# Performance work log

Hardware: AMD Instinct MI355X
Metric: run time of the kernel (lower is better)

The kernel has to match this reference:

```python
import jax, jax.numpy as jnp
import numpy as np

B, IN, OUT, K = 16384, 2048, 2048, 8
P, Q = OUT // K, IN // K
W_BIT, IN_BIT = 8, 8
V_MAX = 2.0
ACT_THRES = 6.0


def _ste(base, quantized):
    # straight-through estimator: forward = quantized, backward = d(base)
    return base + jax.lax.stop_gradient(quantized - base)


def quantize_input(x, in_bit):
    # unsigned uniform quantization of activations into [0, 1]
    levels = float(2 ** in_bit - 1)
    xc = jnp.clip(x, 0.0, 1.0)
    xq = jnp.round(xc * levels) / levels
    return _ste(xc, xq)


def quantize_weight(w, w_bit, v_max):
    # symmetric uniform quantization into [-v_max, v_max]
    s = float(2 ** (w_bit - 1) - 1)
    wc = jnp.clip(w, -v_max, v_max)
    wq = jnp.round(wc / v_max * s) / s * v_max
    return _ste(wc, wq)


def setup_inputs() -> dict:
    key = jax.random.key(0)
    k1, k2 = jax.random.split(key)
    x = jax.random.uniform(k1, (B, IN), dtype=jnp.float32)
    weight = jax.random.normal(k2, (P, Q, K, K), dtype=jnp.float32) * 0.1
    return {"x": x, "weight": weight}


def reference(x, weight):
    xq = quantize_input(x, IN_BIT)                    # [B, IN]
    wq = quantize_weight(weight, W_BIT, V_MAX)        # [P, Q, K, K]
    xb = xq.reshape(x.shape[0], Q, K)                 # [B, Q, K]
    # blocked matmul: out[b,p,o] = sum_q sum_i W[p,q,o,i] * x[b,q,i]
    out = jnp.einsum("bqi,pqoi->bpo", xb, wq).reshape(x.shape[0], OUT)
    out = out * out                                   # photodetect: intensity |.|^2
    out = jnp.clip(out, 0.0, ACT_THRES)               # ReLUN(6)
    return out
```

## Files before the change

kernel.cpp:

```cpp
#include <hip/hip_runtime.h>
#include <stdint.h>


typedef int i32x4  __attribute__((ext_vector_type(4)));
typedef int i32x16 __attribute__((ext_vector_type(16)));

#define B_DIM   16384
#define IN_DIM  2048
#define OUT_DIM 2048

#define BM 256
#define BN 256
#define BK 128
#define KTILES (IN_DIM / BK)
#define ATILE  (BM * BK)
#define BUFB   (2 * ATILE)

__device__ __forceinline__ void async16(const void* g, void* l) {
    __builtin_amdgcn_global_load_lds(
        (const __attribute__((address_space(1))) void*)g,
        (__attribute__((address_space(3))) void*)l, 16, 0, 0);
}

__global__ __launch_bounds__(256) void quant_x_kernel(const float* __restrict__ x,
                                                      int8_t* __restrict__ xq) {
    int i = blockIdx.x * 256 + threadIdx.x;
    const float4* xv = (const float4*)x + (size_t)i * 4;
    union { int8_t c[16]; i32x4 v; } u;
#pragma unroll
    for (int j = 0; j < 4; ++j) {
        float4 v = xv[j];
        float f[4] = {v.x, v.y, v.z, v.w};
#pragma unroll
        for (int e = 0; e < 4; ++e) {
            float c = fminf(fmaxf(f[e], 0.0f), 1.0f);
            int q = (int)rintf(c * 255.0f) - 128;
            u.c[j * 4 + e] = (int8_t)q;
        }
    }
    *((i32x4*)xq + i) = u.v;
}

__global__ __launch_bounds__(256) void quant_w_kernel(const float* __restrict__ w,
                                                      int8_t* __restrict__ wq,
                                                      int* __restrict__ rowsum) {
    int p = blockIdx.x;
    int t = threadIdx.x;
    const float* wp = w + (size_t)p * 16384;
    int n = p * 8 + (t & 7);
    int lsum = 0;
#pragma unroll
    for (int s = 0; s < 8; ++s) {
        int g = t + s * 256;
        float4 v0 = *(const float4*)(wp + g * 8);
        float4 v1 = *(const float4*)(wp + g * 8 + 4);
        float f[8] = {v0.x, v0.y, v0.z, v0.w, v1.x, v1.y, v1.z, v1.w};
        union { int8_t c[8]; long long ll; } u;
#pragma unroll
        for (int e = 0; e < 8; ++e) {
            float c = fminf(fmaxf(f[e], -2.0f), 2.0f);
            int q = (int)rintf(c * 63.5f);
            u.c[e] = (int8_t)q;
            lsum += q;
        }
        int kg = g >> 3;
        *(long long*)(wq + (size_t)n * 2048 + kg * 8) = u.ll;
    }
    atomicAdd(&rowsum[n], lsum);
}

#define LD(p) (*(const i32x4*)(p))
#define MFMA32(a, b, c) __builtin_amdgcn_mfma_i32_32x32x32_i8(a, b, c, 0, 0, 0)

__global__ __launch_bounds__(512, 2) void gemm_i8_kernel(const int8_t* __restrict__ A,
                                                         const int8_t* __restrict__ W,
                                                         const int* __restrict__ rowsum,
                                                         float* __restrict__ out) {
    extern __shared__ int8_t lds[];

    int bid = blockIdx.x;
    int wg = (bid & 7) * 64 + (bid >> 3);
    int tm = wg >> 3;
    int tn = wg & 7;
    int browG = tm * BM;
    int bcolG = tn * BN;

    int tid  = threadIdx.x;
    int lane = tid & 63;
    int wv   = tid >> 6;
    int wr = wv >> 2, wc = wv & 3;
    int l31 = lane & 31;
    int hi  = lane >> 5;

    int csw = (tid & 7) ^ ((tid >> 4) & 7);
    const int8_t* gA = A + (size_t)(browG + (tid >> 3)) * IN_DIM + csw * 16;
    const int8_t* gB = W + (size_t)(bcolG + (tid >> 3)) * IN_DIM + csw * 16;
    const int t16 = tid * 16;

    const int xsw = (l31 >> 1) & 7;
    int kof[4];
#pragma unroll
    for (int ks = 0; ks < 4; ++ks)
        kof[ks] = (((2 * ks + hi) ^ xsw) << 4);
    const int arowO = (wr * 128 + l31) * BK;
    const int browO = (wc * 64 + l31) * BK;

    i32x16 acc[4][2];
#pragma unroll
    for (int m = 0; m < 4; ++m)
#pragma unroll
        for (int n = 0; n < 2; ++n)
            acc[m][n] = (i32x16){0, 0, 0, 0, 0, 0, 0, 0, 0, 0, 0, 0, 0, 0, 0, 0};

    async16(gA, lds + t16);
    async16(gA + 131072, lds + 8192 + t16);
    async16(gA + 262144, lds + 16384 + t16);
    async16(gA + 393216, lds + 24576 + t16);
    async16(gB, lds + ATILE + t16);
    async16(gB + 131072, lds + ATILE + 8192 + t16);
    async16(gB + 262144, lds + ATILE + 16384 + t16);
    async16(gB + 393216, lds + ATILE + 24576 + t16);
    __syncthreads();

#pragma unroll 1
    for (int kt = 0; kt < KTILES; ++kt) {
        const int cur = kt & 1;
        const int8_t* la = lds + cur * BUFB;
        const int8_t* lb = la + ATILE;

        if (kt < KTILES - 1) {
            int8_t* dst = lds + (cur ^ 1) * BUFB;
            const int kb = (kt + 1) * BK;
            async16(gA + kb, dst + t16);
            async16(gA + 131072 + kb, dst + 8192 + t16);
            async16(gA + 262144 + kb, dst + 16384 + t16);
            async16(gA + 393216 + kb, dst + 24576 + t16);
            async16(gB + kb, dst + ATILE + t16);
            async16(gB + 131072 + kb, dst + ATILE + 8192 + t16);
            async16(gB + 262144 + kb, dst + ATILE + 16384 + t16);
            async16(gB + 393216 + kb, dst + ATILE + 24576 + t16);
        }

#pragma unroll
        for (int ks = 0; ks < 4; ++ks) {
            i32x4 a0 = LD(la + arowO + kof[ks]);
            i32x4 a1 = LD(la + arowO + 4096 + kof[ks]);
            i32x4 a2 = LD(la + arowO + 8192 + kof[ks]);
            i32x4 a3 = LD(la + arowO + 12288 + kof[ks]);
            i32x4 b0 = LD(lb + browO + kof[ks]);
            i32x4 b1 = LD(lb + browO + 4096 + kof[ks]);
            acc[0][0] = MFMA32(a0, b0, acc[0][0]);
            acc[0][1] = MFMA32(a0, b1, acc[0][1]);
            acc[1][0] = MFMA32(a1, b0, acc[1][0]);
            acc[1][1] = MFMA32(a1, b1, acc[1][1]);
            acc[2][0] = MFMA32(a2, b0, acc[2][0]);
            acc[2][1] = MFMA32(a2, b1, acc[2][1]);
            acc[3][0] = MFMA32(a3, b0, acc[3][0]);
            acc[3][1] = MFMA32(a3, b1, acc[3][1]);
        }
        __syncthreads();
    }

    const float scale = (float)(2.0 / 32385.0);
#pragma unroll
    for (int n = 0; n < 2; ++n) {
        int col = bcolG + wc * 64 + n * 32 + l31;
        int rs128 = rowsum[col] << 7;
#pragma unroll
        for (int m = 0; m < 4; ++m) {
            int rb = browG + wr * 128 + m * 32 + hi * 4;
#pragma unroll
            for (int r = 0; r < 16; ++r) {
                int row = rb + (r & 3) + 8 * (r >> 2);
                float f = (float)(acc[m][n][r] + rs128) * scale;
                f = f * f;
                f = fminf(f, 6.0f);
                out[(size_t)row * OUT_DIM + col] = f;
            }
        }
    }
}

extern "C" void kernel_launch(void* const* d_in, const int* in_sizes, int n_in,
                              void* d_out, int out_size, void* d_ws, size_t ws_size,
                              hipStream_t stream) {
    const float* x  = (const float*)d_in[0];
    const float* wt = (const float*)d_in[1];
    float* out = (float*)d_out;

    char* ws = (char*)d_ws;
    int8_t* xq = (int8_t*)ws;
    int8_t* wq = (int8_t*)(ws + (size_t)B_DIM * IN_DIM);
    int*    rowsum = (int*)(ws + (size_t)B_DIM * IN_DIM
                               + (size_t)OUT_DIM * IN_DIM);

    hipMemsetAsync(rowsum, 0, OUT_DIM * sizeof(int), stream);
    quant_x_kernel<<<(B_DIM * IN_DIM / 16) / 256, 256, 0, stream>>>(x, xq);
    quant_w_kernel<<<256, 256, 0, stream>>>(wt, wq, rowsum);
    gemm_i8_kernel<<<(B_DIM / BM) * (OUT_DIM / BN), 512, 2 * BUFB, stream>>>(xq, wq, rowsum, out);
}
```

Before: 124.9 us.

## Load weight operand directly into registers from pre-swizzled global layout

Result: slower. 129.3 us (+3.6%).

```diff
diff --git a/kernel.cpp b/kernel.cpp
--- a/kernel.cpp
+++ b/kernel.cpp
@@ -14,7 +14,7 @@
 #define BK 128
 #define KTILES (IN_DIM / BK)
 #define ATILE  (BM * BK)
-#define BUFB   (2 * ATILE)
+#define BUFB   ATILE
 
 __device__ __forceinline__ void async16(const void* g, void* l) {
     __builtin_amdgcn_global_load_lds(
@@ -42,13 +42,13 @@
 }
 
 __global__ __launch_bounds__(256) void quant_w_kernel(const float* __restrict__ w,
-                                                      int8_t* __restrict__ wq,
+                                                      int8_t* __restrict__ wqT,
                                                       int* __restrict__ rowsum) {
     int p = blockIdx.x;
     int t = threadIdx.x;
     const float* wp = w + (size_t)p * 16384;
+    int lsum = 0;
     int n = p * 8 + (t & 7);
-    int lsum = 0;
 #pragma unroll
     for (int s = 0; s < 8; ++s) {
         int g = t + s * 256;
@@ -63,8 +63,7 @@
             u.c[e] = (int8_t)q;
             lsum += q;
         }
-        int kg = g >> 3;
-        *(long long*)(wq + (size_t)n * 2048 + kg * 8) = u.ll;
+        *(long long*)(wqT + ((size_t)(g >> 4) << 15) + n * 16 + ((g >> 3) & 1) * 8) = u.ll;
     }
     atomicAdd(&rowsum[n], lsum);
 }
@@ -73,7 +72,7 @@
 #define MFMA32(a, b, c) __builtin_amdgcn_mfma_i32_32x32x32_i8(a, b, c, 0, 0, 0)
 
 __global__ __launch_bounds__(512, 2) void gemm_i8_kernel(const int8_t* __restrict__ A,
-                                                         const int8_t* __restrict__ W,
+                                                         const int8_t* __restrict__ WT,
                                                          const int* __restrict__ rowsum,
                                                          float* __restrict__ out) {
     extern __shared__ int8_t lds[];
@@ -94,7 +93,6 @@
 
     int csw = (tid & 7) ^ ((tid >> 4) & 7);
     const int8_t* gA = A + (size_t)(browG + (tid >> 3)) * IN_DIM + csw * 16;
-    const int8_t* gB = W + (size_t)(bcolG + (tid >> 3)) * IN_DIM + csw * 16;
     const int t16 = tid * 16;
 
     const int xsw = (l31 >> 1) & 7;
@@ -103,7 +101,8 @@
     for (int ks = 0; ks < 4; ++ks)
         kof[ks] = (((2 * ks + hi) ^ xsw) << 4);
     const int arowO = (wr * 128 + l31) * BK;
-    const int browO = (wc * 64 + l31) * BK;
+
+    const int8_t* gBT = WT + ((size_t)(bcolG + wc * 64 + l31) << 4) + (hi << 15);
 
     i32x16 acc[4][2];
 #pragma unroll
@@ -111,34 +110,30 @@
 #pragma unroll
         for (int n = 0; n < 2; ++n)
             acc[m][n] = (i32x16){0, 0, 0, 0, 0, 0, 0, 0, 0, 0, 0, 0, 0, 0, 0, 0};
+    i32x4 b[2][4];
 
     async16(gA, lds + t16);
     async16(gA + 131072, lds + 8192 + t16);
     async16(gA + 262144, lds + 16384 + t16);
     async16(gA + 393216, lds + 24576 + t16);
-    async16(gB, lds + ATILE + t16);
-    async16(gB + 131072, lds + ATILE + 8192 + t16);
-    async16(gB + 262144, lds + ATILE + 16384 + t16);
-    async16(gB + 393216, lds + ATILE + 24576 + t16);
+#pragma unroll
+    for (int ks = 0; ks < 4; ++ks) {
+        b[0][ks] = LD(gBT + (ks << 16));
+        b[1][ks] = LD(gBT + (ks << 16) + 512);
+    }
     __syncthreads();
 
 #pragma unroll 1
     for (int kt = 0; kt < KTILES; ++kt) {
-        const int cur = kt & 1;
-        const int8_t* la = lds + cur * BUFB;
-        const int8_t* lb = la + ATILE;
+        const int8_t* la = lds + (kt & 1) * BUFB;
 
         if (kt < KTILES - 1) {
-            int8_t* dst = lds + (cur ^ 1) * BUFB;
+            int8_t* dst = lds + ((kt & 1) ^ 1) * BUFB;
             const int kb = (kt + 1) * BK;
             async16(gA + kb, dst + t16);
             async16(gA + 131072 + kb, dst + 8192 + t16);
             async16(gA + 262144 + kb, dst + 16384 + t16);
             async16(gA + 393216 + kb, dst + 24576 + t16);
-            async16(gB + kb, dst + ATILE + t16);
-            async16(gB + 131072 + kb, dst + ATILE + 8192 + t16);
-            async16(gB + 262144 + kb, dst + ATILE + 16384 + t16);
-            async16(gB + 393216 + kb, dst + ATILE + 24576 + t16);
         }
 
 #pragma unroll
@@ -147,16 +142,23 @@
             i32x4 a1 = LD(la + arowO + 4096 + kof[ks]);
             i32x4 a2 = LD(la + arowO + 8192 + kof[ks]);
             i32x4 a3 = LD(la + arowO + 12288 + kof[ks]);
-            i32x4 b0 = LD(lb + browO + kof[ks]);
-            i32x4 b1 = LD(lb + browO + 4096 + kof[ks]);
-            acc[0][0] = MFMA32(a0, b0, acc[0][0]);
-            acc[0][1] = MFMA32(a0, b1, acc[0][1]);
-            acc[1][0] = MFMA32(a1, b0, acc[1][0]);
-            acc[1][1] = MFMA32(a1, b1, acc[1][1]);
-            acc[2][0] = MFMA32(a2, b0, acc[2][0]);
-            acc[2][1] = MFMA32(a2, b1, acc[2][1]);
-            acc[3][0] = MFMA32(a3, b0, acc[3][0]);
-            acc[3][1] = MFMA32(a3, b1, acc[3][1]);
+            acc[0][0] = MFMA32(a0, b[0][ks], acc[0][0]);
+            acc[0][1] = MFMA32(a0, b[1][ks], acc[0][1]);
+            acc[1][0] = MFMA32(a1, b[0][ks], acc[1][0]);
+            acc[1][1] = MFMA32(a1, b[1][ks], acc[1][1]);
+            acc[2][0] = MFMA32(a2, b[0][ks], acc[2][0]);
+            acc[2][1] = MFMA32(a2, b[1][ks], acc[2][1]);
+            acc[3][0] = MFMA32(a3, b[0][ks], acc[3][0]);
+            acc[3][1] = MFMA32(a3, b[1][ks], acc[3][1]);
+        }
+
+        if (kt < KTILES - 1) {
+            const size_t kb = (size_t)(kt + 1) << 18;
+#pragma unroll
+            for (int ks = 0; ks < 4; ++ks) {
+                b[0][ks] = LD(gBT + kb + (ks << 16));
+                b[1][ks] = LD(gBT + kb + (ks << 16) + 512);
+            }
         }
         __syncthreads();
     }
@@ -189,13 +191,13 @@
     float* out = (float*)d_out;
 
     char* ws = (char*)d_ws;
-    int8_t* xq = (int8_t*)ws;
-    int8_t* wq = (int8_t*)(ws + (size_t)B_DIM * IN_DIM);
+    int8_t* xq  = (int8_t*)ws;
+    int8_t* wqT = (int8_t*)(ws + (size_t)B_DIM * IN_DIM);
     int*    rowsum = (int*)(ws + (size_t)B_DIM * IN_DIM
                                + (size_t)OUT_DIM * IN_DIM);
 
     hipMemsetAsync(rowsum, 0, OUT_DIM * sizeof(int), stream);
     quant_x_kernel<<<(B_DIM * IN_DIM / 16) / 256, 256, 0, stream>>>(x, xq);
-    quant_w_kernel<<<256, 256, 0, stream>>>(wt, wq, rowsum);
-    gemm_i8_kernel<<<(B_DIM / BM) * (OUT_DIM / BN), 512, 2 * BUFB, stream>>>(xq, wq, rowsum, out);
-}
+    quant_w_kernel<<<256, 256, 0, stream>>>(wt, wqT, rowsum);
+    gemm_i8_kernel<<<(B_DIM / BM) * (OUT_DIM / BN), 512, 2 * BUFB, stream>>>(xq, wqT, rowsum, out);
+}
```

## Pre-transpose quantized operands to chunk-major layout and load MFMA fragments from global

Applied to the files above, without the earlier changes.

New measurement: 144.7 us. +15.9%, slower.

```diff
diff --git a/kernel.cpp b/kernel.cpp
--- a/kernel.cpp
+++ b/kernel.cpp
@@ -13,42 +13,53 @@
 #define BN 256
 #define BK 128
 #define KTILES (IN_DIM / BK)
-#define ATILE  (BM * BK)
-#define BUFB   (2 * ATILE)
+#define AKC ((size_t)B_DIM * 16)
+#define BKC ((size_t)OUT_DIM * 16)
 
-__device__ __forceinline__ void async16(const void* g, void* l) {
-    __builtin_amdgcn_global_load_lds(
-        (const __attribute__((address_space(1))) void*)g,
-        (__attribute__((address_space(3))) void*)l, 16, 0, 0);
+__device__ __forceinline__ int q4(float4 v) {
+    int a = (int)rintf(fminf(fmaxf(v.x, 0.f), 1.f) * 255.f) - 128;
+    int b = (int)rintf(fminf(fmaxf(v.y, 0.f), 1.f) * 255.f) - 128;
+    int c = (int)rintf(fminf(fmaxf(v.z, 0.f), 1.f) * 255.f) - 128;
+    int d = (int)rintf(fminf(fmaxf(v.w, 0.f), 1.f) * 255.f) - 128;
+    return (a & 255) | ((b & 255) << 8) | ((c & 255) << 16) | ((d & 255) << 24);
 }
 
 __global__ __launch_bounds__(256) void quant_x_kernel(const float* __restrict__ x,
-                                                      int8_t* __restrict__ xq) {
-    int i = blockIdx.x * 256 + threadIdx.x;
-    const float4* xv = (const float4*)x + (size_t)i * 4;
-    union { int8_t c[16]; i32x4 v; } u;
+                                                      int8_t* __restrict__ xqT) {
+    __shared__ int8_t sm[64 * 272];
+    int bid = blockIdx.x;
+    int b0 = (bid >> 3) * 64;
+    int kc0 = (bid & 7) * 16;
+    int t = threadIdx.x;
+
+    int rl = t >> 2;
+    const float* xr = x + (size_t)(b0 + rl) * IN_DIM + (size_t)kc0 * 16 + (t & 3) * 16;
 #pragma unroll
-    for (int j = 0; j < 4; ++j) {
-        float4 v = xv[j];
-        float f[4] = {v.x, v.y, v.z, v.w};
+    for (int s = 0; s < 4; ++s) {
+        const float4* p = (const float4*)(xr + s * 64);
+        i32x4 pk;
+        pk[0] = q4(p[0]); pk[1] = q4(p[1]); pk[2] = q4(p[2]); pk[3] = q4(p[3]);
+        *(i32x4*)(sm + rl * 272 + ((t & 3) + 4 * s) * 16) = pk;
+    }
+    __syncthreads();
+
+    int bl = t & 63, w = t >> 6;
 #pragma unroll
-        for (int e = 0; e < 4; ++e) {
-            float c = fminf(fmaxf(f[e], 0.0f), 1.0f);
-            int q = (int)rintf(c * 255.0f) - 128;
-            u.c[j * 4 + e] = (int8_t)q;
-        }
+    for (int s = 0; s < 4; ++s) {
+        int kcl = s * 4 + w;
+        i32x4 v = *(const i32x4*)(sm + bl * 272 + kcl * 16);
+        *(i32x4*)(xqT + (size_t)(kc0 + kcl) * AKC + (size_t)(b0 + bl) * 16) = v;
     }
-    *((i32x4*)xq + i) = u.v;
 }
 
 __global__ __launch_bounds__(256) void quant_w_kernel(const float* __restrict__ w,
-                                                      int8_t* __restrict__ wq,
+                                                      int8_t* __restrict__ wqT,
                                                       int* __restrict__ rowsum) {
     int p = blockIdx.x;
     int t = threadIdx.x;
     const float* wp = w + (size_t)p * 16384;
+    int lsum = 0;
     int n = p * 8 + (t & 7);
-    int lsum = 0;
 #pragma unroll
     for (int s = 0; s < 8; ++s) {
         int g = t + s * 256;
@@ -63,8 +74,7 @@
             u.c[e] = (int8_t)q;
             lsum += q;
         }
-        int kg = g >> 3;
-        *(long long*)(wq + (size_t)n * 2048 + kg * 8) = u.ll;
+        *(long long*)(wqT + ((size_t)(g >> 4) << 15) + n * 16 + ((g >> 3) & 1) * 8) = u.ll;
     }
     atomicAdd(&rowsum[n], lsum);
 }
@@ -72,12 +82,10 @@
 #define LD(p) (*(const i32x4*)(p))
 #define MFMA32(a, b, c) __builtin_amdgcn_mfma_i32_32x32x32_i8(a, b, c, 0, 0, 0)
 
-__global__ __launch_bounds__(512, 2) void gemm_i8_kernel(const int8_t* __restrict__ A,
-                                                         const int8_t* __restrict__ W,
+__global__ __launch_bounds__(512, 2) void gemm_i8_kernel(const int8_t* __restrict__ AT,
+                                                         const int8_t* __restrict__ WT,
                                                          const int* __restrict__ rowsum,
                                                          float* __restrict__ out) {
-    extern __shared__ int8_t lds[];
-
     int bid = blockIdx.x;
     int wg = (bid & 7) * 64 + (bid >> 3);
     int tm = wg >> 3;
@@ -92,18 +100,8 @@
     int l31 = lane & 31;
     int hi  = lane >> 5;
 
-    int csw = (tid & 7) ^ ((tid >> 4) & 7);
-    const int8_t* gA = A + (size_t)(browG + (tid >> 3)) * IN_DIM + csw * 16;
-    const int8_t* gB = W + (size_t)(bcolG + (tid >> 3)) * IN_DIM + csw * 16;
-    const int t16 = tid * 16;
-
-    const int xsw = (l31 >> 1) & 7;
-    int kof[4];
-#pragma unroll
-    for (int ks = 0; ks < 4; ++ks)
-        kof[ks] = (((2 * ks + hi) ^ xsw) << 4);
-    const int arowO = (wr * 128 + l31) * BK;
-    const int browO = (wc * 64 + l31) * BK;
+    const int8_t* gAT = AT + (size_t)hi * AKC + ((size_t)(browG + wr * 128 + l31) << 4);
+    const int8_t* gBT = WT + (size_t)hi * BKC + ((size_t)(bcolG + wc * 64 + l31) << 4);
 
     i32x16 acc[4][2];
 #pragma unroll
@@ -112,43 +110,20 @@
         for (int n = 0; n < 2; ++n)
             acc[m][n] = (i32x16){0, 0, 0, 0, 0, 0, 0, 0, 0, 0, 0, 0, 0, 0, 0, 0};
 
-    async16(gA, lds + t16);
-    async16(gA + 131072, lds + 8192 + t16);
-    async16(gA + 262144, lds + 16384 + t16);
-    async16(gA + 393216, lds + 24576 + t16);
-    async16(gB, lds + ATILE + t16);
-    async16(gB + 131072, lds + ATILE + 8192 + t16);
-    async16(gB + 262144, lds + ATILE + 16384 + t16);
-    async16(gB + 393216, lds + ATILE + 24576 + t16);
-    __syncthreads();
-
 #pragma unroll 1
     for (int kt = 0; kt < KTILES; ++kt) {
-        const int cur = kt & 1;
-        const int8_t* la = lds + cur * BUFB;
-        const int8_t* lb = la + ATILE;
-
-        if (kt < KTILES - 1) {
-            int8_t* dst = lds + (cur ^ 1) * BUFB;
-            const int kb = (kt + 1) * BK;
-            async16(gA + kb, dst + t16);
-            async16(gA + 131072 + kb, dst + 8192 + t16);
-            async16(gA + 262144 + kb, dst + 16384 + t16);
-            async16(gA + 393216 + kb, dst + 24576 + t16);
-            async16(gB + kb, dst + ATILE + t16);
-            async16(gB + 131072 + kb, dst + ATILE + 8192 + t16);
-            async16(gB + 262144 + kb, dst + ATILE + 16384 + t16);
-            async16(gB + 393216 + kb, dst + ATILE + 24576 + t16);
-        }
-
+        const int8_t* pa = gAT + (size_t)kt * (8 * AKC);
+        const int8_t* pb = gBT + (size_t)kt * (8 * BKC);
 #pragma unroll
         for (int ks = 0; ks < 4; ++ks) {
-            i32x4 a0 = LD(la + arowO + kof[ks]);
-            i32x4 a1 = LD(la + arowO + 4096 + kof[ks]);
-            i32x4 a2 = LD(la + arowO + 8192 + kof[ks]);
-            i32x4 a3 = LD(la + arowO + 12288 + kof[ks]);
-            i32x4 b0 = LD(lb + browO + kof[ks]);
-            i32x4 b1 = LD(lb + browO + 4096 + kof[ks]);
+            const int8_t* qa = pa + (size_t)ks * (2 * AKC);
+            const int8_t* qb = pb + (size_t)ks * (2 * BKC);
+            i32x4 a0 = LD(qa);
+            i32x4 a1 = LD(qa + 512);
+            i32x4 a2 = LD(qa + 1024);
+            i32x4 a3 = LD(qa + 1536);
+            i32x4 b0 = LD(qb);
+            i32x4 b1 = LD(qb + 512);
             acc[0][0] = MFMA32(a0, b0, acc[0][0]);
             acc[0][1] = MFMA32(a0, b1, acc[0][1]);
             acc[1][0] = MFMA32(a1, b0, acc[1][0]);
@@ -158,7 +133,6 @@
             acc[3][0] = MFMA32(a3, b0, acc[3][0]);
             acc[3][1] = MFMA32(a3, b1, acc[3][1]);
         }
-        __syncthreads();
     }
 
     const float scale = (float)(2.0 / 32385.0);
@@ -189,13 +163,13 @@
     float* out = (float*)d_out;
 
     char* ws = (char*)d_ws;
-    int8_t* xq = (int8_t*)ws;
-    int8_t* wq = (int8_t*)(ws + (size_t)B_DIM * IN_DIM);
+    int8_t* xqT = (int8_t*)ws;
+    int8_t* wqT = (int8_t*)(ws + (size_t)B_DIM * IN_DIM);
     int*    rowsum = (int*)(ws + (size_t)B_DIM * IN_DIM
                                + (size_t)OUT_DIM * IN_DIM);
 
     hipMemsetAsync(rowsum, 0, OUT_DIM * sizeof(int), stream);
-    quant_x_kernel<<<(B_DIM * IN_DIM / 16) / 256, 256, 0, stream>>>(x, xq);
-    quant_w_kernel<<<256, 256, 0, stream>>>(wt, wq, rowsum);
-    gemm_i8_kernel<<<(B_DIM / BM) * (OUT_DIM / BN), 512, 2 * BUFB, stream>>>(xq, wq, rowsum, out);
+    quant_x_kernel<<<(B_DIM / 64) * (IN_DIM / 256), 256, 0, stream>>>(x, xqT);
+    quant_w_kernel<<<256, 256, 0, stream>>>(wt, wqT, rowsum);
+    gemm_i8_kernel<<<(B_DIM / BM) * (OUT_DIM / BN), 512, 0, stream>>>(xqT, wqT, rowsum, out);
 }
```

## Shrink GEMM tiles to 128x256x64 for higher occupancy and drop rowsum memset

Applied to the files above, without the earlier changes.

Measured after the change: 126.2 us. No clear change (+1.1%).

```diff
diff --git a/kernel.cpp b/kernel.cpp
--- a/kernel.cpp
+++ b/kernel.cpp
@@ -9,12 +9,13 @@
 #define IN_DIM  2048
 #define OUT_DIM 2048
 
-#define BM 256
+#define BM 128
 #define BN 256
-#define BK 128
+#define BK 64
 #define KTILES (IN_DIM / BK)
 #define ATILE  (BM * BK)
-#define BUFB   (2 * ATILE)
+#define BTILE  (BN * BK)
+#define BUFB   (ATILE + BTILE)
 
 __device__ __forceinline__ void async16(const void* g, void* l) {
     __builtin_amdgcn_global_load_lds(
@@ -44,6 +45,7 @@
 __global__ __launch_bounds__(256) void quant_w_kernel(const float* __restrict__ w,
                                                       int8_t* __restrict__ wq,
                                                       int* __restrict__ rowsum) {
+    __shared__ int smsum[256];
     int p = blockIdx.x;
     int t = threadIdx.x;
     const float* wp = w + (size_t)p * 16384;
@@ -66,20 +68,27 @@
         int kg = g >> 3;
         *(long long*)(wq + (size_t)n * 2048 + kg * 8) = u.ll;
     }
-    atomicAdd(&rowsum[n], lsum);
+    smsum[t] = lsum;
+    __syncthreads();
+    if (t < 8) {
+        int s = 0;
+#pragma unroll
+        for (int j = 0; j < 32; ++j) s += smsum[t + j * 8];
+        rowsum[p * 8 + t] = s;
+    }
 }
 
 #define LD(p) (*(const i32x4*)(p))
 #define MFMA32(a, b, c) __builtin_amdgcn_mfma_i32_32x32x32_i8(a, b, c, 0, 0, 0)
 
-__global__ __launch_bounds__(512, 2) void gemm_i8_kernel(const int8_t* __restrict__ A,
+__global__ __launch_bounds__(512, 4) void gemm_i8_kernel(const int8_t* __restrict__ A,
                                                          const int8_t* __restrict__ W,
                                                          const int* __restrict__ rowsum,
                                                          float* __restrict__ out) {
     extern __shared__ int8_t lds[];
 
     int bid = blockIdx.x;
-    int wg = (bid & 7) * 64 + (bid >> 3);
+    int wg = (bid & 7) * 128 + (bid >> 3);
     int tm = wg >> 3;
     int tn = wg & 7;
     int browG = tm * BM;
@@ -92,71 +101,61 @@
     int l31 = lane & 31;
     int hi  = lane >> 5;
 
-    int csw = (tid & 7) ^ ((tid >> 4) & 7);
-    const int8_t* gA = A + (size_t)(browG + (tid >> 3)) * IN_DIM + csw * 16;
-    const int8_t* gB = W + (size_t)(bcolG + (tid >> 3)) * IN_DIM + csw * 16;
+    int csw = (tid & 3) ^ ((tid >> 3) & 3);
+    const int8_t* gA = A + (size_t)(browG + (tid >> 2)) * IN_DIM + csw * 16;
+    const int8_t* gB = W + (size_t)(bcolG + (tid >> 2)) * IN_DIM + csw * 16;
     const int t16 = tid * 16;
 
-    const int xsw = (l31 >> 1) & 7;
-    int kof[4];
-#pragma unroll
-    for (int ks = 0; ks < 4; ++ks)
-        kof[ks] = (((2 * ks + hi) ^ xsw) << 4);
-    const int arowO = (wr * 128 + l31) * BK;
+    const int xsw = (l31 >> 1) & 3;
+    const int kof0 = (((0 + hi) ^ xsw) << 4);
+    const int kof1 = (((2 + hi) ^ xsw) << 4);
+    const int arowO = (wr * 64 + l31) * BK;
     const int browO = (wc * 64 + l31) * BK;
 
-    i32x16 acc[4][2];
+    i32x16 acc[2][2];
 #pragma unroll
-    for (int m = 0; m < 4; ++m)
+    for (int m = 0; m < 2; ++m)
 #pragma unroll
         for (int n = 0; n < 2; ++n)
             acc[m][n] = (i32x16){0, 0, 0, 0, 0, 0, 0, 0, 0, 0, 0, 0, 0, 0, 0, 0};
 
     async16(gA, lds + t16);
-    async16(gA + 131072, lds + 8192 + t16);
-    async16(gA + 262144, lds + 16384 + t16);
-    async16(gA + 393216, lds + 24576 + t16);
     async16(gB, lds + ATILE + t16);
-    async16(gB + 131072, lds + ATILE + 8192 + t16);
-    async16(gB + 262144, lds + ATILE + 16384 + t16);
-    async16(gB + 393216, lds + ATILE + 24576 + t16);
+    async16(gB + 262144, lds + ATILE + 8192 + t16);
     __syncthreads();
 
 #pragma unroll 1
     for (int kt = 0; kt < KTILES; ++kt) {
-        const int cur = kt & 1;
-        const int8_t* la = lds + cur * BUFB;
+        const int8_t* la = lds + (kt & 1) * BUFB;
         const int8_t* lb = la + ATILE;
 
         if (kt < KTILES - 1) {
-            int8_t* dst = lds + (cur ^ 1) * BUFB;
+            int8_t* dst = lds + ((kt & 1) ^ 1) * BUFB;
             const int kb = (kt + 1) * BK;
             async16(gA + kb, dst + t16);
-            async16(gA + 131072 + kb, dst + 8192 + t16);
-            async16(gA + 262144 + kb, dst + 16384 + t16);
-            async16(gA + 393216 + kb, dst + 24576 + t16);
             async16(gB + kb, dst + ATILE + t16);
-            async16(gB + 131072 + kb, dst + ATILE + 8192 + t16);
-            async16(gB + 262144 + kb, dst + ATILE + 16384 + t16);
-            async16(gB + 393216 + kb, dst + ATILE + 24576 + t16);
+            async16(gB + 262144 + kb, dst + ATILE + 8192 + t16);
         }
 
-#pragma unroll
-        for (int ks = 0; ks < 4; ++ks) {
-            i32x4 a0 = LD(la + arowO + kof[ks]);
-            i32x4 a1 = LD(la + arowO + 4096 + kof[ks]);
-            i32x4 a2 = LD(la + arowO + 8192 + kof[ks]);
-            i32x4 a3 = LD(la + arowO + 12288 + kof[ks]);
-            i32x4 b0 = LD(lb + browO + kof[ks]);
-            i32x4 b1 = LD(lb + browO + 4096 + kof[ks]);
+        {
+            i32x4 a0 = LD(la + arowO + kof0);
+            i32x4 a1 = LD(la + arowO + 2048 + kof0);
+            i32x4 b0 = LD(lb + browO + kof0);
+            i32x4 b1 = LD(lb + browO + 2048 + kof0);
             acc[0][0] = MFMA32(a0, b0, acc[0][0]);
             acc[0][1] = MFMA32(a0, b1, acc[0][1]);
             acc[1][0] = MFMA32(a1, b0, acc[1][0]);
             acc[1][1] = MFMA32(a1, b1, acc[1][1]);
-            acc[2][0] = MFMA32(a2, b0, acc[2][0]);
-            acc[2][1] = MFMA32(a2, b1, acc[2][1]);
-            acc[3][0] = MFMA32(a3, b0, acc[3][0]);
-            acc[3][1] = MFMA32(a3, b1, acc[3][1]);
+        }
+        {
+            i32x4 a0 = LD(la + arowO + kof1);
+            i32x4 a1 = LD(la + arowO + 2048 + kof1);
+            i32x4 b0 = LD(lb + browO + kof1);
+            i32x4 b1 = LD(lb + browO + 2048 + kof1);
+            acc[0][0] = MFMA32(a0, b0, acc[0][0]);
+            acc[0][1] = MFMA32(a0, b1, acc[0][1]);
+            acc[1][0] = MFMA32(a1, b0, acc[1][0]);
+            acc[1][1] = MFMA32(a1, b1, acc[1][1]);
         }
         __syncthreads();
     }
@@ -167,8 +166,8 @@
         int col = bcolG + wc * 64 + n * 32 + l31;
         int rs128 = rowsum[col] << 7;
 #pragma unroll
-        for (int m = 0; m < 4; ++m) {
-            int rb = browG + wr * 128 + m * 32 + hi * 4;
+        for (int m = 0; m < 2; ++m) {
+            int rb = browG + wr * 64 + m * 32 + hi * 4;
 #pragma unroll
             for (int r = 0; r < 16; ++r) {
                 int row = rb + (r & 3) + 8 * (r >> 2);
@@ -194,7 +193,6 @@
     int*    rowsum = (int*)(ws + (size_t)B_DIM * IN_DIM
                                + (size_t)OUT_DIM * IN_DIM);
 
-    hipMemsetAsync(rowsum, 0, OUT_DIM * sizeof(int), stream);
     quant_x_kernel<<<(B_DIM * IN_DIM / 16) / 256, 256, 0, stream>>>(x, xq);
     quant_w_kernel<<<256, 256, 0, stream>>>(wt, wq, rowsum);
     gemm_i8_kernel<<<(B_DIM / BM) * (OUT_DIM / BN), 512, 2 * BUFB, stream>>>(xq, wq, rowsum, out);
```
